# Optimization experiments

Measured on AMD Instinct MI355X. Metric: run time of the kernel, lower is better.

The kernel has to match this reference:

```python
import jax, jax.numpy as jnp
import numpy as np


def _squash(s, axis=-1, eps=1e-8):
    # squash(s) = |s|^2/(1+|s|^2) * s/|s|
    s2 = jnp.sum(s * s, axis=axis, keepdims=True)
    return (s2 / (1.0 + s2)) * s / jnp.sqrt(s2 + eps)


def _conv(x, w, b, stride):
    y = jax.lax.conv_general_dilated(
        x, w, (stride, stride), 'VALID',
        dimension_numbers=('NCHW', 'OIHW', 'NCHW'))
    return y + b[None, :, None, None]


def setup_inputs() -> dict:
    key = jax.random.key(0)
    ks = jax.random.split(key, 4)
    B = 64
    sc = 0.05
    return {
        'x': jax.random.normal(ks[0], (B, 3, 32, 32), jnp.float32),
        'conv_w': jax.random.normal(ks[1], (256, 3, 9, 9), jnp.float32) * sc,
        'conv_b': jnp.zeros((256,), jnp.float32),
        'pcap_w': jax.random.normal(ks[2], (256, 256, 9, 9), jnp.float32) * sc,
        'pcap_b': jnp.zeros((256,), jnp.float32),
        'W': jax.random.normal(ks[3], (100, 2048, 16, 8), jnp.float32) * sc,
    }


def reference(x, conv_w, conv_b, pcap_w, pcap_b, W):
    # Conv stem: [B,3,32,32] -> [B,256,24,24]
    h = jax.nn.relu(_conv(x, conv_w, conv_b, 1))
    # PrimaryCaps conv: [B,256,24,24] -> [B,256,8,8], then view to capsules
    p = _conv(h, pcap_w, pcap_b, 2)
    u = _squash(p.reshape(p.shape[0], 2048, 8))            # [B,2048,8]
    # DenseCapsule: u_hat[b,o,i,d] = W[o,i,d,k] u[b,i,k]
    u_hat = jnp.einsum('oidk,bik->boid', W, u)             # [B,100,2048,16]
    u_hat_sg = jax.lax.stop_gradient(u_hat)
    b = jnp.zeros(u_hat.shape[:3], u_hat.dtype)            # [B,100,2048]
    routings = 3
    v = None
    for i in range(routings):
        c = jax.nn.softmax(b, axis=1)                      # over out caps
        uh = u_hat if i == routings - 1 else u_hat_sg
        v = _squash(jnp.einsum('boi,boid->bod', c, uh))    # [B,100,16]
        if i < routings - 1:
            b = b + jnp.einsum('bod,boid->boi', v, u_hat_sg)
    return v
```

## Files before the change

kernel.cpp:

```cpp
#include <hip/hip_runtime.h>

#define NB 64
#define NO 100
#define NI 2048
#define ND 16
#define NK 8

#define WS_H    0
#define WS_U    9437184
#define WS_BB   10485760
#define WS_CB   23592960
#define WS_SP   36700160
#define WS_V    38338560
#define WS_PP   WS_BB

typedef __attribute__((ext_vector_type(8))) short bf16x8;
typedef __attribute__((ext_vector_type(16))) float f32x16;
typedef __attribute__((ext_vector_type(4))) float f32x4;

__device__ inline unsigned short f2bf(float x) {
    union { float f; unsigned u; } v; v.f = x;
    unsigned r = (v.u + 0x7FFFu + ((v.u >> 16) & 1u)) >> 16;
    return (unsigned short)r;
}
__device__ inline float bf2f(unsigned short h) {
    union { unsigned u; float f; } v; v.u = ((unsigned)h) << 16;
    return v.f;
}

__global__ __launch_bounds__(256) void conv1_kernel(const float* __restrict__ x,
        const float* __restrict__ w, const float* __restrict__ bias,
        unsigned short* __restrict__ h_hi, unsigned short* __restrict__ h_lo) {
    const int b = blockIdx.x;
    const int ocg = blockIdx.y;
    __shared__ float xl[3 * 32 * 32];
    __shared__ float wl[16 * 243];
    const int tid = threadIdx.x;
    for (int idx = tid; idx < 3072; idx += 256) xl[idx] = x[b * 3072 + idx];
    for (int idx = tid; idx < 16 * 243; idx += 256)
        wl[idx] = w[ocg * 16 * 243 + idx];
    __syncthreads();
    const int lane = tid & 63;
    const int wg = tid >> 6;
    float acc[4][9];
    #pragma unroll
    for (int jj = 0; jj < 4; ++jj) {
        float bv = bias[ocg * 16 + wg * 4 + jj];
        #pragma unroll
        for (int j = 0; j < 9; ++j) acc[jj][j] = bv;
    }
    int xbase[9];
    #pragma unroll
    for (int j = 0; j < 9; ++j) {
        int p = lane + 64 * j;
        xbase[j] = (p / 24) * 32 + (p % 24);
    }
    for (int ic = 0; ic < 3; ++ic)
        for (int ky = 0; ky < 9; ++ky) {
            #pragma unroll
            for (int kx = 0; kx < 9; ++kx) {
                float wv[4];
                #pragma unroll
                for (int jj = 0; jj < 4; ++jj)
                    wv[jj] = wl[(wg * 4 + jj) * 243 + ic * 81 + ky * 9 + kx];
                #pragma unroll
                for (int j = 0; j < 9; ++j) {
                    float xv = xl[ic * 1024 + xbase[j] + ky * 32 + kx];
                    #pragma unroll
                    for (int jj = 0; jj < 4; ++jj)
                        acc[jj][j] = fmaf(xv, wv[jj], acc[jj][j]);
                }
            }
        }
    #pragma unroll
    for (int jj = 0; jj < 4; ++jj) {
        int oc = ocg * 16 + wg * 4 + jj;
        #pragma unroll
        for (int j = 0; j < 9; ++j) {
            int p = lane + 64 * j;
            float v = fmaxf(acc[jj][j], 0.f);
            unsigned short hi = f2bf(v);
            unsigned short lo = f2bf(v - bf2f(hi));
            size_t o = (size_t)(b * 256 + oc) * 576 + p;
            h_hi[o] = hi;
            h_lo[o] = lo;
        }
    }
}

__global__ __launch_bounds__(256) void wb_precompute_kernel(const float* __restrict__ w,
        unsigned short* __restrict__ wBhi, unsigned short* __restrict__ wBlo) {
    const int ic = blockIdx.x;
    const int ocq = blockIdx.y;
    __shared__ float tl[64][85];
    const int tid = threadIdx.x;
    for (int f = tid; f < 5184; f += 256) {
        int oc = f / 81, kk = f % 81;
        tl[oc][kk] = w[(size_t)(ocq * 64 + oc) * 20736 + ic * 81 + kk];
    }
    __syncthreads();
    for (int idx = tid; idx < 9216; idx += 256) {
        int ky = idx >> 10;
        int rem = idx & 1023;
        int ocl = rem >> 4;
        int kx = rem & 15;
        float val = (kx < 9) ? tl[ocl][ky * 9 + kx] : 0.f;
        unsigned short hi = f2bf(val);
        unsigned short lo = f2bf(val - bf2f(hi));
        size_t dst = ((size_t)(ic * 9 + ky) * 256 + ocq * 64 + ocl) * 16 + kx;
        wBhi[dst] = hi;
        wBlo[dst] = lo;
    }
}

__global__ __launch_bounds__(256) void conv2_mfma_kernel(
        const unsigned short* __restrict__ h_hi, const unsigned short* __restrict__ h_lo,
        const unsigned short* __restrict__ wBhi, const unsigned short* __restrict__ wBlo,
        float* __restrict__ pp) {
    const int b = blockIdx.x;
    const int ocb = blockIdx.y;
    const int ks = blockIdx.z;
    __shared__ __align__(16) unsigned short Bh[2][64 * 16];
    __shared__ __align__(16) unsigned short Bl[2][64 * 16];
    const int tid = threadIdx.x;
    const int lane = tid & 63;
    const int wid = tid >> 6;
    const int wr = wid >> 1, wc = wid & 1;
    const int l31 = lane & 31, kh = lane >> 5;
    const int slot = tid & 63;
    const int role = (tid >> 6) & 1;
    const int oy = slot >> 3;
    const int ox = slot & 7;
    const unsigned short* hsel = role ? h_lo : h_hi;
    const size_t hrow0 = (size_t)b * 256 * 576;
    const int ic0 = ks * 32;

    const int aoff0 = (wr * 64 + l31) * 16 + kh * 8;
    const int aoff1 = aoff0 + 512;
    const int boff = (wc * 32 + l31) * 16 + kh * 8;

    f32x16 acc[2];
    #pragma unroll
    for (int m = 0; m < 2; ++m)
        #pragma unroll
        for (int r = 0; r < 16; ++r) acc[m][r] = 0.f;

    unsigned int d0, d1, d2, d3, d4;

#define GLOADB(c) if (tid < 128) { const int ic_ = ic0 + (c) / 9, ky_ = (c) % 9;           \
    const unsigned int* hp_ = (const unsigned int*)(hsel + hrow0 + (size_t)ic_ * 576       \
        + (2 * oy + ky_) * 24 + 2 * ox);                                                   \
    d0 = hp_[0]; d1 = hp_[1]; d2 = hp_[2]; d3 = hp_[3]; d4 = hp_[4]; }
#define STOREB(buf) if (tid < 128) {                                                       \
    unsigned short* Bdst_ = (role ? Bl[buf] : Bh[buf]) + slot * 16;                        \
    uint4 w0_; w0_.x = d0; w0_.y = d1; w0_.z = d2; w0_.w = d3;                             \
    uint4 w1_; w1_.x = d4 & 0xFFFFu; w1_.y = 0u; w1_.z = 0u; w1_.w = 0u;                   \
    *(uint4*)Bdst_ = w0_; *(uint4*)(Bdst_ + 8) = w1_; }
#define LOADA(c, AH, AL) { const int ic_ = ic0 + (c) / 9, ky_ = (c) % 9;                   \
    const size_t base_ = (size_t)ic_ * 36864 + (size_t)ky_ * 4096 + ocb * 2048;            \
    AH[0] = *(const bf16x8*)(wBhi + base_ + aoff0);                                        \
    AH[1] = *(const bf16x8*)(wBhi + base_ + aoff1);                                        \
    AL[0] = *(const bf16x8*)(wBlo + base_ + aoff0);                                        \
    AL[1] = *(const bf16x8*)(wBlo + base_ + aoff1); }
#define MFMA6(AH, AL, buf) {                                                               \
    bf16x8 bh0 = *(const bf16x8*)&Bh[buf][boff];                                           \
    bf16x8 bl0 = *(const bf16x8*)&Bl[buf][boff];                                           \
    acc[0] = __builtin_amdgcn_mfma_f32_32x32x16_bf16(AH[0], bh0, acc[0], 0, 0, 0);         \
    acc[0] = __builtin_amdgcn_mfma_f32_32x32x16_bf16(AH[0], bl0, acc[0], 0, 0, 0);         \
    acc[0] = __builtin_amdgcn_mfma_f32_32x32x16_bf16(AL[0], bh0, acc[0], 0, 0, 0);         \
    acc[1] = __builtin_amdgcn_mfma_f32_32x32x16_bf16(AH[1], bh0, acc[1], 0, 0, 0);         \
    acc[1] = __builtin_amdgcn_mfma_f32_32x32x16_bf16(AH[1], bl0, acc[1], 0, 0, 0);         \
    acc[1] = __builtin_amdgcn_mfma_f32_32x32x16_bf16(AL[1], bh0, acc[1], 0, 0, 0); }

    bf16x8 a0h[2], a0l[2], a1h[2], a1l[2];
    GLOADB(0); STOREB(0);
    GLOADB(1);
    LOADA(0, a0h, a0l);
    __syncthreads();
    #pragma unroll 1
    for (int c = 0; c < 288; c += 2) {
        LOADA(c + 1, a1h, a1l);
        MFMA6(a0h, a0l, 0);
        STOREB(1);
        if (c + 2 < 288) GLOADB(c + 2);
        __syncthreads();
        if (c + 2 < 288) LOADA(c + 2, a0h, a0l);
        MFMA6(a1h, a1l, 1);
        if (c + 2 < 288) {
            STOREB(0);
            GLOADB(c + 3);
        }
        __syncthreads();
    }
#undef GLOADB
#undef STOREB
#undef LOADA
#undef MFMA6

    #pragma unroll
    for (int m = 0; m < 2; ++m) {
        const int pos = wc * 32 + l31;
        #pragma unroll
        for (int r = 0; r < 16; ++r) {
            const int row = (r & 3) + 8 * (r >> 2) + 4 * kh;
            const int oc = ocb * 128 + wr * 64 + m * 32 + row;
            pp[(((size_t)ks * 64 + b) * 256 + oc) * 64 + pos] = acc[m][r];
        }
    }
}

__global__ __launch_bounds__(256) void reduce_bias_squash_kernel(
        const float* __restrict__ pp, const float* __restrict__ bias,
        float* __restrict__ u) {
    const int cap = blockIdx.x * 256 + threadIdx.x;
    const int b = cap >> 11;
    const int rem = cap & 2047;
    const int oc = rem >> 3;
    const int oy = rem & 7;
    float4 sa = {0.f, 0.f, 0.f, 0.f}, sb = {0.f, 0.f, 0.f, 0.f};
    #pragma unroll
    for (int ks = 0; ks < 8; ++ks) {
        const float4* p4 = (const float4*)&pp[(((size_t)ks * 64 + b) * 256 + oc) * 64 + oy * 8];
        float4 a = p4[0], c = p4[1];
        sa.x += a.x; sa.y += a.y; sa.z += a.z; sa.w += a.w;
        sb.x += c.x; sb.y += c.y; sb.z += c.z; sb.w += c.w;
    }
    const float bv = bias[oc];
    sa.x += bv; sa.y += bv; sa.z += bv; sa.w += bv;
    sb.x += bv; sb.y += bv; sb.z += bv; sb.w += bv;
    float s2 = sa.x * sa.x + sa.y * sa.y + sa.z * sa.z + sa.w * sa.w
             + sb.x * sb.x + sb.y * sb.y + sb.z * sb.z + sb.w * sb.w;
    float scale = (s2 / (1.f + s2)) / sqrtf(s2 + 1e-8f);
    sa.x *= scale; sa.y *= scale; sa.z *= scale; sa.w *= scale;
    sb.x *= scale; sb.y *= scale; sb.z *= scale; sb.w *= scale;
    float4* up = (float4*)&u[(size_t)cap * 8];
    up[0] = sa;
    up[1] = sb;
}

__global__ __launch_bounds__(256) void transpose_u_kernel(const float* __restrict__ u,
        float* __restrict__ ut) {
    const int blk = blockIdx.x;
    __shared__ float tl[64 * 132];
    const int tid = threadIdx.x;
    #pragma unroll
    for (int rep = 0; rep < 8; ++rep) {
        const int idx = tid + 256 * rep;
        const int b = idx >> 5, q = idx & 31;
        float4 uv = *(const float4*)(u + (size_t)b * 16384 + blk * 128 + 4 * q);
        *(float4*)&tl[b * 132 + 4 * q] = uv;
    }
    __syncthreads();
    #pragma unroll
    for (int rep = 0; rep < 32; ++rep) {
        const int row = rep * 4 + (tid >> 6);
        const int b = tid & 63;
        ut[(size_t)(blk * 128 + row) * 64 + b] = tl[b * 132 + row];
    }
}

template <int UNIFORM>
__global__ __launch_bounds__(256) void r_weighted_mfma_kernel(
        const float* __restrict__ W, const float* __restrict__ u,
        const float* __restrict__ cbuf, float* __restrict__ sp) {
    const int o = blockIdx.x;
    const int st = blockIdx.y;
    __shared__ __align__(16) unsigned short Ahi[16 * 72];
    __shared__ __align__(16) unsigned short Alo[16 * 72];
    __shared__ __align__(16) unsigned short Bhi[64 * 72];
    __shared__ __align__(16) unsigned short Blo[64 * 72];
    const int tid = threadIdx.x;
    const int lane = tid & 63;
    const int w = tid >> 6;
    const int l15 = lane & 15;
    const int hi = lane >> 4;
    const int sb = tid >> 2;
    const int si = tid & 3;
    f32x4 acc = {0.f, 0.f, 0.f, 0.f};
    const float* Wo = W + (size_t)o * 262144;
    const int i_base = st * 256;
    #pragma unroll 1
    for (int iter = 0; iter < 32; ++iter) {
        const int i0 = i_base + iter * 8;
        __syncthreads();
        {
            float4 wv = *(const float4*)(Wo + (size_t)i0 * 128 + 4 * tid);
            const int i_l = tid >> 5;
            const int d = (tid >> 1) & 15;
            const int k0 = (tid & 1) * 4;
            unsigned short* dh = Ahi + d * 72 + i_l * 8 + k0;
            unsigned short* dl = Alo + d * 72 + i_l * 8 + k0;
            float vv[4] = {wv.x, wv.y, wv.z, wv.w};
            unsigned int h01, h23, l01, l23;
            unsigned short h, l;
            h = f2bf(vv[0]); l = f2bf(vv[0] - bf2f(h)); h01 = h; l01 = l;
            h = f2bf(vv[1]); l = f2bf(vv[1] - bf2f(h)); h01 |= (unsigned)h << 16; l01 |= (unsigned)l << 16;
            h = f2bf(vv[2]); l = f2bf(vv[2] - bf2f(h)); h23 = h; l23 = l;
            h = f2bf(vv[3]); l = f2bf(vv[3] - bf2f(h)); h23 |= (unsigned)h << 16; l23 |= (unsigned)l << 16;
            *(unsigned int*)dh = h01; *(unsigned int*)(dh + 2) = h23;
            *(unsigned int*)dl = l01; *(unsigned int*)(dl + 2) = l23;
        }
        #pragma unroll
        for (int half = 0; half < 2; ++half) {
            const int i_l = si + 4 * half;
            const float* up = u + (size_t)sb * 16384 + (size_t)(i0 + i_l) * 8;
            float4 u0 = *(const float4*)up;
            float4 u1 = *(const float4*)(up + 4);
            float cv = UNIFORM ? 0.01f
                               : cbuf[(size_t)sb * (NO * NI) + o * NI + i0 + i_l];
            float q[8] = {u0.x * cv, u0.y * cv, u0.z * cv, u0.w * cv,
                          u1.x * cv, u1.y * cv, u1.z * cv, u1.w * cv};
            uint4 ph, pl;
            unsigned short h0, h1, l0, l1;
            h0 = f2bf(q[0]); l0 = f2bf(q[0] - bf2f(h0));
            h1 = f2bf(q[1]); l1 = f2bf(q[1] - bf2f(h1));
            ph.x = h0 | ((unsigned)h1 << 16); pl.x = l0 | ((unsigned)l1 << 16);
            h0 = f2bf(q[2]); l0 = f2bf(q[2] - bf2f(h0));
            h1 = f2bf(q[3]); l1 = f2bf(q[3] - bf2f(h1));
            ph.y = h0 | ((unsigned)h1 << 16); pl.y = l0 | ((unsigned)l1 << 16);
            h0 = f2bf(q[4]); l0 = f2bf(q[4] - bf2f(h0));
            h1 = f2bf(q[5]); l1 = f2bf(q[5] - bf2f(h1));
            ph.z = h0 | ((unsigned)h1 << 16); pl.z = l0 | ((unsigned)l1 << 16);
            h0 = f2bf(q[6]); l0 = f2bf(q[6] - bf2f(h0));
            h1 = f2bf(q[7]); l1 = f2bf(q[7] - bf2f(h1));
            ph.w = h0 | ((unsigned)h1 << 16); pl.w = l0 | ((unsigned)l1 << 16);
            *(uint4*)(Bhi + sb * 72 + i_l * 8) = ph;
            *(uint4*)(Blo + sb * 72 + i_l * 8) = pl;
        }
        __syncthreads();
        #pragma unroll
        for (int ch = 0; ch < 2; ++ch) {
            bf16x8 ah = *(const bf16x8*)(Ahi + l15 * 72 + ch * 32 + hi * 8);
            bf16x8 al = *(const bf16x8*)(Alo + l15 * 72 + ch * 32 + hi * 8);
            bf16x8 bh = *(const bf16x8*)(Bhi + (w * 16 + l15) * 72 + ch * 32 + hi * 8);
            bf16x8 bl = *(const bf16x8*)(Blo + (w * 16 + l15) * 72 + ch * 32 + hi * 8);
            acc = __builtin_amdgcn_mfma_f32_16x16x32_bf16(ah, bh, acc, 0, 0, 0);
            acc = __builtin_amdgcn_mfma_f32_16x16x32_bf16(ah, bl, acc, 0, 0, 0);
            acc = __builtin_amdgcn_mfma_f32_16x16x32_bf16(al, bh, acc, 0, 0, 0);
        }
    }
    const int bg = w * 16 + l15;
    float4 st4;
    st4.x = acc[0]; st4.y = acc[1]; st4.z = acc[2]; st4.w = acc[3];
    *(float4*)&sp[(((size_t)o * 8 + st) * 64 + bg) * 16 + hi * 4] = st4;
}

__global__ __launch_bounds__(256) void squash_v_kernel(const float* __restrict__ sp,
        float* __restrict__ dest) {
    const int t = blockIdx.x * 256 + threadIdx.x;
    const int d = t & 15;
    const int cap = t >> 4;
    const int o = cap >> 6;
    const int bb = cap & 63;
    float s = 0.f;
    #pragma unroll
    for (int st = 0; st < 8; ++st)
        s += sp[(((size_t)o * 8 + st) * 64 + bb) * 16 + d];
    float s2 = s * s;
    #pragma unroll
    for (int off = 1; off < 16; off <<= 1)
        s2 += __shfl_xor(s2, off, 16);
    float scale = (s2 / (1.f + s2)) / sqrtf(s2 + 1e-8f);
    dest[(bb * NO + o) * ND + d] = s * scale;
}

template <int ADD>
__global__ __launch_bounds__(256) void r_logits_mfma_kernel(
        const float* __restrict__ W, const float* __restrict__ ut,
        const float* __restrict__ v, float* __restrict__ bbuf) {
    const int o = blockIdx.x;
    const int st = blockIdx.y;
    __shared__ __align__(16) unsigned short Aext[128 * 40];
    __shared__ __align__(16) unsigned short B1[64 * 40];
    __shared__ __align__(16) unsigned short B2[64 * 40];
    __shared__ float ul[128 * 66];
    const int tid = threadIdx.x;
    const int lane = tid & 63;
    const int w = tid >> 6;
    const int l15 = lane & 15;
    const int hi = lane >> 4;
    const float* Wo = W + (size_t)o * 262144;
    {
        const int b = tid >> 2;
        const int dq = (tid & 3) * 4;
        float4 vv = *(const float4*)&v[((size_t)b * NO + o) * ND + dq];
        float q[4] = {vv.x, vv.y, vv.z, vv.w};
        #pragma unroll
        for (int c = 0; c < 4; ++c) {
            unsigned short h = f2bf(q[c]);
            unsigned short l = f2bf(q[c] - bf2f(h));
            B1[b * 40 + dq + c] = h;
            B1[b * 40 + 16 + dq + c] = h;
            B2[b * 40 + dq + c] = l;
            B2[b * 40 + 16 + dq + c] = 0;
        }
    }
    __syncthreads();
    #pragma unroll 1
    for (int iter = 0; iter < 8; ++iter) {
        __syncthreads();
        #pragma unroll
        for (int rep = 0; rep < 2; ++rep) {
            const int off = 4 * tid + 1024 * rep;
            float4 wv = *(const float4*)(Wo + (size_t)(st * 128 + iter * 16) * 128 + off);
            const int i_l = off >> 7;
            const int d = (off >> 3) & 15;
            const int k0 = off & 7;
            float va[4] = {wv.x, wv.y, wv.z, wv.w};
            #pragma unroll
            for (int c = 0; c < 4; ++c) {
                unsigned short h = f2bf(va[c]);
                unsigned short l = f2bf(va[c] - bf2f(h));
                const int row = i_l * 8 + k0 + c;
                Aext[row * 40 + d] = h;
                Aext[row * 40 + 16 + d] = l;
            }
        }
        const int base_row = (st * 128 + iter * 16) * 8;
        #pragma unroll
        for (int rep = 0; rep < 8; ++rep) {
            const int idx = tid + 256 * rep;
            const int row = idx >> 4, bq = idx & 15;
            float4 uv = *(const float4*)(ut + (size_t)(base_row + row) * 64 + 4 * bq);
            *(float4*)&ul[row * 66 + 4 * bq] = uv;
        }
        __syncthreads();
        f32x4 acc[8];
        bf16x8 bf1 = *(const bf16x8*)&B1[(w * 16 + l15) * 40 + hi * 8];
        bf16x8 bf2 = *(const bf16x8*)&B2[(w * 16 + l15) * 40 + hi * 8];
        #pragma unroll
        for (int mt = 0; mt < 8; ++mt) {
            f32x4 z = {0.f, 0.f, 0.f, 0.f};
            bf16x8 af = *(const bf16x8*)&Aext[(mt * 16 + l15) * 40 + hi * 8];
            z = __builtin_amdgcn_mfma_f32_16x16x32_bf16(af, bf1, z, 0, 0, 0);
            z = __builtin_amdgcn_mfma_f32_16x16x32_bf16(af, bf2, z, 0, 0, 0);
            acc[mt] = z;
        }
        #pragma unroll
        for (int mt = 0; mt < 8; ++mt) {
            float partial = 0.f;
            #pragma unroll
            for (int r = 0; r < 4; ++r) {
                const int grow = mt * 16 + hi * 4 + r;
                partial = fmaf(acc[mt][r], ul[grow * 66 + w * 16 + l15], partial);
            }
            float sum = partial + __shfl_xor(partial, 16);
            if ((hi & 1) == 0) {
                const int i_glob = st * 128 + iter * 16 + mt * 2 + (hi >> 1);
                const int bg = w * 16 + l15;
                const size_t addr = (size_t)bg * (NO * NI) + (size_t)o * NI + i_glob;
                bbuf[addr] = (ADD ? bbuf[addr] : 0.f) + sum;
            }
        }
    }
}

__global__ __launch_bounds__(256) void softmax_kernel(const float* __restrict__ bbuf,
        float* __restrict__ cbuf) {
    const int bb = blockIdx.x >> 3;
    const int i = (blockIdx.x & 7) * 256 + threadIdx.x;
    const float* col = bbuf + bb * (NO * NI) + i;
    float m = -1e30f;
    for (int o = 0; o < NO; ++o) m = fmaxf(m, col[o * NI]);
    float s = 0.f;
    for (int o = 0; o < NO; ++o) s += __expf(col[o * NI] - m);
    const float inv = 1.f / s;
    float* outp = cbuf + bb * (NO * NI) + i;
    for (int o = 0; o < NO; ++o) outp[o * NI] = __expf(col[o * NI] - m) * inv;
}

extern "C" void kernel_launch(void* const* d_in, const int* in_sizes, int n_in,
                              void* d_out, int out_size, void* d_ws, size_t ws_size,
                              hipStream_t stream) {
    (void)in_sizes; (void)n_in; (void)out_size; (void)ws_size;
    const float* x      = (const float*)d_in[0];
    const float* conv_w = (const float*)d_in[1];
    const float* conv_b = (const float*)d_in[2];
    const float* pcap_w = (const float*)d_in[3];
    const float* pcap_b = (const float*)d_in[4];
    const float* W      = (const float*)d_in[5];
    float* out = (float*)d_out;
    float* ws  = (float*)d_ws;
    unsigned short* h_hi = (unsigned short*)(ws + WS_H);
    unsigned short* h_lo = h_hi + 9437184;
    unsigned short* wBhi = (unsigned short*)(ws + WS_CB);
    unsigned short* wBlo = wBhi + 9437184;
    float* ut  = ws + WS_H;
    float* u   = ws + WS_U;
    float* bbf = ws + WS_BB;
    float* cbf = ws + WS_CB;
    float* sp  = ws + WS_SP;
    float* v   = ws + WS_V;
    float* pp  = ws + WS_PP;

    wb_precompute_kernel<<<dim3(256, 4), 256, 0, stream>>>(pcap_w, wBhi, wBlo);
    conv1_kernel<<<dim3(64, 16), 256, 0, stream>>>(x, conv_w, conv_b, h_hi, h_lo);
    conv2_mfma_kernel<<<dim3(64, 2, 8), 256, 0, stream>>>(h_hi, h_lo, wBhi, wBlo, pp);
    reduce_bias_squash_kernel<<<512, 256, 0, stream>>>(pp, pcap_b, u);
    transpose_u_kernel<<<128, 256, 0, stream>>>(u, ut);
    r_weighted_mfma_kernel<1><<<dim3(100, 8), 256, 0, stream>>>(W, u, nullptr, sp);
    squash_v_kernel<<<400, 256, 0, stream>>>(sp, v);
    r_logits_mfma_kernel<0><<<dim3(100, 16), 256, 0, stream>>>(W, ut, v, bbf);
    softmax_kernel<<<512, 256, 0, stream>>>(bbf, cbf);
    r_weighted_mfma_kernel<0><<<dim3(100, 8), 256, 0, stream>>>(W, u, cbf, sp);
    squash_v_kernel<<<400, 256, 0, stream>>>(sp, v);
    r_logits_mfma_kernel<1><<<dim3(100, 16), 256, 0, stream>>>(W, ut, v, bbf);
    softmax_kernel<<<512, 256, 0, stream>>>(bbf, cbf);
    r_weighted_mfma_kernel<0><<<dim3(100, 8), 256, 0, stream>>>(W, u, cbf, sp);
    squash_v_kernel<<<400, 256, 0, stream>>>(sp, out);
}
```

Baseline: 859.5 us.

## Load conv2 B operands directly from global, dropping LDS staging and barriers

The primary-caps conv MFMA kernel no longer stages the im2col input patches in a double-buffered LDS tile with __syncthreads. Each lane now reads its own B fragment straight from global memory (hi and lo bf16 planes) and zeroes the upper half for the kh lanes. This removes the barriers and the LDS round trip. In exchange there are more redundant global loads across waves, and the loop loses its explicit software prefetch, so load latency relies on unrolling and occupancy.

After: 878.9 us. +2.3%, slower.

```diff
diff --git a/kernel.cpp b/kernel.cpp
--- a/kernel.cpp
+++ b/kernel.cpp
@@ -120,24 +120,18 @@
     const int b = blockIdx.x;
     const int ocb = blockIdx.y;
     const int ks = blockIdx.z;
-    __shared__ __align__(16) unsigned short Bh[2][64 * 16];
-    __shared__ __align__(16) unsigned short Bl[2][64 * 16];
     const int tid = threadIdx.x;
     const int lane = tid & 63;
     const int wid = tid >> 6;
     const int wr = wid >> 1, wc = wid & 1;
     const int l31 = lane & 31, kh = lane >> 5;
-    const int slot = tid & 63;
-    const int role = (tid >> 6) & 1;
-    const int oy = slot >> 3;
-    const int ox = slot & 7;
-    const unsigned short* hsel = role ? h_lo : h_hi;
-    const size_t hrow0 = (size_t)b * 256 * 576;
+    const int pos = wc * 32 + l31;
+    const int oy = pos >> 3, ox = pos & 7;
     const int ic0 = ks * 32;
 
-    const int aoff0 = (wr * 64 + l31) * 16 + kh * 8;
-    const int aoff1 = aoff0 + 512;
-    const int boff = (wc * 32 + l31) * 16 + kh * 8;
+    const size_t abase = (size_t)ocb * 2048 + (size_t)(wr * 64 + l31) * 16 + kh * 8;
+    const size_t hplane0 = (size_t)b * 147456 + (size_t)ic0 * 576;
+    const int boffs = 2 * ox + kh * 8;
 
     f32x16 acc[2];
     #pragma unroll
@@ -145,61 +139,46 @@
         #pragma unroll
         for (int r = 0; r < 16; ++r) acc[m][r] = 0.f;
 
-    unsigned int d0, d1, d2, d3, d4;
-
-#define GLOADB(c) if (tid < 128) { const int ic_ = ic0 + (c) / 9, ky_ = (c) % 9;           \
-    const unsigned int* hp_ = (const unsigned int*)(hsel + hrow0 + (size_t)ic_ * 576       \
-        + (2 * oy + ky_) * 24 + 2 * ox);                                                   \
-    d0 = hp_[0]; d1 = hp_[1]; d2 = hp_[2]; d3 = hp_[3]; d4 = hp_[4]; }
-#define STOREB(buf) if (tid < 128) {                                                       \
-    unsigned short* Bdst_ = (role ? Bl[buf] : Bh[buf]) + slot * 16;                        \
-    uint4 w0_; w0_.x = d0; w0_.y = d1; w0_.z = d2; w0_.w = d3;                             \
-    uint4 w1_; w1_.x = d4 & 0xFFFFu; w1_.y = 0u; w1_.z = 0u; w1_.w = 0u;                   \
-    *(uint4*)Bdst_ = w0_; *(uint4*)(Bdst_ + 8) = w1_; }
-#define LOADA(c, AH, AL) { const int ic_ = ic0 + (c) / 9, ky_ = (c) % 9;                   \
-    const size_t base_ = (size_t)ic_ * 36864 + (size_t)ky_ * 4096 + ocb * 2048;            \
-    AH[0] = *(const bf16x8*)(wBhi + base_ + aoff0);                                        \
-    AH[1] = *(const bf16x8*)(wBhi + base_ + aoff1);                                        \
-    AL[0] = *(const bf16x8*)(wBlo + base_ + aoff0);                                        \
-    AL[1] = *(const bf16x8*)(wBlo + base_ + aoff1); }
-#define MFMA6(AH, AL, buf) {                                                               \
-    bf16x8 bh0 = *(const bf16x8*)&Bh[buf][boff];                                           \
-    bf16x8 bl0 = *(const bf16x8*)&Bl[buf][boff];                                           \
-    acc[0] = __builtin_amdgcn_mfma_f32_32x32x16_bf16(AH[0], bh0, acc[0], 0, 0, 0);         \
-    acc[0] = __builtin_amdgcn_mfma_f32_32x32x16_bf16(AH[0], bl0, acc[0], 0, 0, 0);         \
-    acc[0] = __builtin_amdgcn_mfma_f32_32x32x16_bf16(AL[0], bh0, acc[0], 0, 0, 0);         \
-    acc[1] = __builtin_amdgcn_mfma_f32_32x32x16_bf16(AH[1], bh0, acc[1], 0, 0, 0);         \
-    acc[1] = __builtin_amdgcn_mfma_f32_32x32x16_bf16(AH[1], bl0, acc[1], 0, 0, 0);         \
-    acc[1] = __builtin_amdgcn_mfma_f32_32x32x16_bf16(AL[1], bh0, acc[1], 0, 0, 0); }
-
-    bf16x8 a0h[2], a0l[2], a1h[2], a1l[2];
-    GLOADB(0); STOREB(0);
-    GLOADB(1);
-    LOADA(0, a0h, a0l);
-    __syncthreads();
     #pragma unroll 1
-    for (int c = 0; c < 288; c += 2) {
-        LOADA(c + 1, a1h, a1l);
-        MFMA6(a0h, a0l, 0);
-        STOREB(1);
-        if (c + 2 < 288) GLOADB(c + 2);
-        __syncthreads();
-        if (c + 2 < 288) LOADA(c + 2, a0h, a0l);
-        MFMA6(a1h, a1l, 1);
-        if (c + 2 < 288) {
-            STOREB(0);
-            GLOADB(c + 3);
-        }
-        __syncthreads();
-    }
-#undef GLOADB
-#undef STOREB
-#undef LOADA
-#undef MFMA6
+    for (int ic_l = 0; ic_l < 32; ++ic_l) {
+        const size_t wbase = (size_t)(ic0 + ic_l) * 36864 + abase;
+        const size_t hbase = hplane0 + (size_t)ic_l * 576;
+        #pragma unroll 3
+        for (int ky = 0; ky < 9; ++ky) {
+            const size_t wk = wbase + (size_t)ky * 4096;
+            bf16x8 ah0 = *(const bf16x8*)(wBhi + wk);
+            bf16x8 ah1 = *(const bf16x8*)(wBhi + wk + 512);
+            bf16x8 al0 = *(const bf16x8*)(wBlo + wk);
+            bf16x8 al1 = *(const bf16x8*)(wBlo + wk + 512);
+            const unsigned short* ph = h_hi + hbase + (2 * oy + ky) * 24 + boffs;
+            const unsigned short* pl = h_lo + hbase + (2 * oy + ky) * 24 + boffs;
+            uint4 rh, rl;
+            rh.x = *(const unsigned int*)(ph);
+            rh.y = *(const unsigned int*)(ph + 2);
+            rh.z = *(const unsigned int*)(ph + 4);
+            rh.w = *(const unsigned int*)(ph + 6);
+            rl.x = *(const unsigned int*)(pl);
+            rl.y = *(const unsigned int*)(pl + 2);
+            rl.z = *(const unsigned int*)(pl + 4);
+            rl.w = *(const unsigned int*)(pl + 6);
+            if (kh) {
+                rh.x &= 0xFFFFu; rh.y = 0u; rh.z = 0u; rh.w = 0u;
+                rl.x &= 0xFFFFu; rl.y = 0u; rl.z = 0u; rl.w = 0u;
+            }
+            union { uint4 u; bf16x8 v; } cvh, cvl;
+            cvh.u = rh; cvl.u = rl;
+            bf16x8 bh = cvh.v, bl = cvl.v;
+            acc[0] = __builtin_amdgcn_mfma_f32_32x32x16_bf16(ah0, bh, acc[0], 0, 0, 0);
+            acc[0] = __builtin_amdgcn_mfma_f32_32x32x16_bf16(ah0, bl, acc[0], 0, 0, 0);
+            acc[0] = __builtin_amdgcn_mfma_f32_32x32x16_bf16(al0, bh, acc[0], 0, 0, 0);
+            acc[1] = __builtin_amdgcn_mfma_f32_32x32x16_bf16(ah1, bh, acc[1], 0, 0, 0);
+            acc[1] = __builtin_amdgcn_mfma_f32_32x32x16_bf16(ah1, bl, acc[1], 0, 0, 0);
+            acc[1] = __builtin_amdgcn_mfma_f32_32x32x16_bf16(al1, bh, acc[1], 0, 0, 0);
+        }
+    }
 
     #pragma unroll
     for (int m = 0; m < 2; ++m) {
-        const int pos = wc * 32 + l31;
         #pragma unroll
         for (int r = 0; r < 16; ++r) {
             const int row = (r & 3) + 8 * (r >> 2) + 4 * kh;
```
